# Kernel optimization log

Hardware: AMD Instinct MI355X
Metric: run time of the kernel (lower is better)

The kernel has to match this reference:

```python
import jax, jax.numpy as jnp
import numpy as np

SEQ, B, D = 2048, 16, 1024  # seq_len, batch, input/hidden size

def setup_inputs() -> dict:
    key = jax.random.key(0)
    k1, k2, k3 = jax.random.split(key, 3)
    X = jax.random.normal(k1, (SEQ, B, D), dtype=jnp.float32)
    hidden = jnp.zeros((B, D), dtype=jnp.float32)  # initial hidden state C_0
    # nn.Linear(window*input_size, 3*hidden_size): weight (3D, D), bias (3D,)
    W = jax.random.normal(k2, (3 * D, D), dtype=jnp.float32) / np.float32(np.sqrt(D))
    b = jax.random.normal(k3, (3 * D,), dtype=jnp.float32) * 0.01
    return {"X": X, "hidden": hidden, "W": W, "b": b}

def _forget_mult(F, Z, h0):
    # C_t = F_t * Z_t + (1 - F_t) * C_{t-1}, scanned over seq dim
    def step(h, fz):
        f, z = fz
        h = f * z + (1.0 - f) * h
        return h, h
    _, C = jax.lax.scan(step, h0, (F, Z))
    return C  # (S, B, D)

def reference(X, hidden, W, b):
    # window=1 -> source = X; gate projection
    Y = jnp.einsum('sbd,hd->sbh', X, W) + b        # (S, B, 3D)
    Z, F, O = jnp.split(Y, 3, axis=2)
    Z = jnp.tanh(Z)
    F = jax.nn.sigmoid(F)
    C = _forget_mult(F, Z, hidden)                 # (S, B, D)
    H = jax.nn.sigmoid(O) * C                      # output gate (QRNN-fo)
    return H, C[-1:]                               # (S,B,D), (1,B,D)
```

## Files before the change

kernel.cpp:

```cpp
#include <hip/hip_runtime.h>


#define S_LEN 2048
#define BATCH 16
#define DHID 1024
#define N3 3072
#define MROWS (S_LEN * BATCH)
#define XELEMS ((size_t)MROWS * DHID)
#define WELEMS ((size_t)N3 * DHID)
#define YELEMS ((size_t)MROWS * N3)

typedef __attribute__((ext_vector_type(8))) short bf16x8;
typedef __attribute__((ext_vector_type(4))) float floatx4;
typedef __attribute__((ext_vector_type(4))) unsigned short u16x4;

__device__ __forceinline__ float b2f(unsigned short u) {
  return __uint_as_float(((unsigned)u) << 16);
}
__device__ __forceinline__ unsigned short f2b(float x) {
  unsigned u = __float_as_uint(x);
  u += 0x7fffu + ((u >> 16) & 1u);
  return (unsigned short)(u >> 16);
}
__device__ __forceinline__ float sigmoid_f(float x) {
  return __builtin_amdgcn_rcpf(1.0f + __expf(-x));
}
__device__ __forceinline__ float tanh_f(float x) {
  return 2.0f * __builtin_amdgcn_rcpf(1.0f + __expf(-2.0f * x)) - 1.0f;
}

__device__ __forceinline__ void load_lds16(const unsigned short* g, unsigned short* l) {
  __builtin_amdgcn_global_load_lds(
      (const __attribute__((address_space(1))) void*)g,
      (__attribute__((address_space(3))) void*)l,
      16, 0, 0);
}

__global__ __launch_bounds__(256) void cvt_f32_bf16(
    const float* __restrict__ src, unsigned short* __restrict__ dst, int n4) {
  int i = blockIdx.x * 256 + threadIdx.x;
  if (i < n4) {
    float4 v = ((const float4*)src)[i];
    u16x4 o;
    o.x = f2b(v.x); o.y = f2b(v.y); o.z = f2b(v.z); o.w = f2b(v.w);
    ((u16x4*)dst)[i] = o;
  }
}

__global__ __launch_bounds__(256) void qrnn_gemm(
    const unsigned short* __restrict__ X,
    const unsigned short* __restrict__ W,
    const float* __restrict__ bias,
    unsigned short* __restrict__ Y)
{
  __shared__ __align__(16) unsigned short sA[128 * 64];
  __shared__ __align__(16) unsigned short sB[128 * 64];

  const int tid = threadIdx.x;
  const int w  = tid >> 6;
  const int l  = tid & 63;
  const int lr = l & 15;
  const int lq = l >> 4;
  const int n0B = blockIdx.x * 128;
  const int m0B = blockIdx.y * 128;
  const int wm = (w >> 1) * 64;
  const int wn = (w & 1) * 64;

  floatx4 acc[4][4] = {};

  const unsigned short* gA = X + (size_t)m0B * DHID;
  const unsigned short* gB = W + (size_t)n0B * DHID;
  const int srow = tid >> 3;
  const int scol = (tid & 7) << 3;

  for (int k0 = 0; k0 < DHID; k0 += 64) {
#pragma unroll
    for (int j = 0; j < 4; ++j) {
      load_lds16(gA + (size_t)(j * 32 + srow) * DHID + (k0 + scol),
                 sA + (j * 2048 + w * 512));
      load_lds16(gB + (size_t)(j * 32 + srow) * DHID + (k0 + scol),
                 sB + (j * 2048 + w * 512));
    }
    __syncthreads();

#pragma unroll
    for (int kk = 0; kk < 64; kk += 32) {
      bf16x8 af[4], bf[4];
#pragma unroll
      for (int i = 0; i < 4; ++i) {
        af[i] = *(const bf16x8*)&sA[(wm + i * 16 + lr) * 64 + kk + lq * 8];
      }
#pragma unroll
      for (int j = 0; j < 4; ++j) {
        bf[j] = *(const bf16x8*)&sB[(wn + j * 16 + lr) * 64 + kk + lq * 8];
      }
#pragma unroll
      for (int i = 0; i < 4; ++i) {
#pragma unroll
        for (int j = 0; j < 4; ++j) {
          acc[i][j] = __builtin_amdgcn_mfma_f32_16x16x32_bf16(
              af[i], bf[j], acc[i][j], 0, 0, 0);
        }
      }
    }
    __syncthreads();
  }

  const int seg = n0B >> 10;
#pragma unroll
  for (int j = 0; j < 4; ++j) {
    const int n = n0B + wn + j * 16 + lr;
    const float bv = bias[n];
#pragma unroll
    for (int i = 0; i < 4; ++i) {
      const int mb = m0B + wm + i * 16 + lq * 4;
#pragma unroll
      for (int r = 0; r < 4; ++r) {
        float v = acc[i][j][r] + bv;
        v = (seg == 0) ? tanh_f(v) : sigmoid_f(v);
        Y[(size_t)(mb + r) * N3 + n] = f2b(v);
      }
    }
  }
}

#define U 8
#define PCH 32
#define LCH (S_LEN / PCH)
#define SUBCH (LCH / U)
#define SSTRIDE (BATCH * N3)
#define HSTRIDE (BATCH * DHID)
#define NT (BATCH * DHID)
#define NT4 (NT / 4)

__global__ __launch_bounds__(256) void qrnn_scan_pass1(
    const unsigned short* __restrict__ Y,
    float* __restrict__ Aarr,
    float* __restrict__ Barr)
{
  const int g = blockIdx.x * 256 + threadIdx.x;
  const int t = g & (NT4 - 1);
  const int p = g >> 12;
  const int b = t >> 8;
  const int d = (t & 255) << 2;
  const unsigned short* base =
      Y + (size_t)(p * LCH) * SSTRIDE + (size_t)b * N3 + d;

  float a[4] = {1.0f, 1.0f, 1.0f, 1.0f};
  float bv[4] = {0.0f, 0.0f, 0.0f, 0.0f};
  u16x4 z0[U], f0[U], z1[U], f1[U];

#define LOADZF(ch, zz, ff) { \
    const unsigned short* p_ = base + (size_t)(ch) * ((size_t)U * SSTRIDE); \
    _Pragma("unroll") \
    for (int j2 = 0; j2 < U; ++j2) { \
      zz[j2] = *(const u16x4*)(p_ + (size_t)j2 * SSTRIDE); \
      ff[j2] = *(const u16x4*)(p_ + (size_t)j2 * SSTRIDE + DHID); \
    } }

#define COMPAB(zz, ff) { \
    _Pragma("unroll") \
    for (int j2 = 0; j2 < U; ++j2) { \
      _Pragma("unroll") \
      for (int q = 0; q < 4; ++q) { \
        float zv = b2f(zz[j2][q]); \
        float fv = b2f(ff[j2][q]); \
        a[q]  = fmaf(-fv, a[q], a[q]);         \
        bv[q] = fmaf(fv, zv - bv[q], bv[q]);   \
      } \
    } }

  LOADZF(0, z0, f0);
  for (int ch = 0; ch < SUBCH; ch += 2) {
    LOADZF(ch + 1, z1, f1);
    COMPAB(z0, f0);
    if (ch + 2 < SUBCH) LOADZF(ch + 2, z0, f0);
    COMPAB(z1, f1);
  }
  ((float4*)Aarr)[g] = make_float4(a[0], a[1], a[2], a[3]);
  ((float4*)Barr)[g] = make_float4(bv[0], bv[1], bv[2], bv[3]);
}

__global__ __launch_bounds__(256) void qrnn_combine(
    const float* __restrict__ Aarr,
    const float* __restrict__ Barr,
    const float* __restrict__ h0,
    float* __restrict__ Cin,
    float* __restrict__ out)
{
  const int t = blockIdx.x * 256 + threadIdx.x;
  float c = h0[t];
#pragma unroll
  for (int p = 0; p < PCH; ++p) {
    Cin[p * NT + t] = c;
    c = fmaf(Aarr[p * NT + t], c, Barr[p * NT + t]);
  }
  out[(size_t)S_LEN * HSTRIDE + t] = c;
}

__global__ __launch_bounds__(256) void qrnn_scan_pass2(
    const unsigned short* __restrict__ Y,
    const float* __restrict__ Cin,
    float* __restrict__ out)
{
  const int g = blockIdx.x * 256 + threadIdx.x;
  const int t = g & (NT4 - 1);
  const int p = g >> 12;
  const int b = t >> 8;
  const int d = (t & 255) << 2;
  const unsigned short* base =
      Y + (size_t)(p * LCH) * SSTRIDE + (size_t)b * N3 + d;
  float* ho = out + (size_t)(p * LCH) * HSTRIDE + (size_t)b * DHID + d;

  float4 cv = ((const float4*)Cin)[g];
  float c[4] = {cv.x, cv.y, cv.z, cv.w};

  u16x4 z0[U], f0[U], o0[U], z1[U], f1[U], o1[U];

#define LOADCH(ch, zz, ff, oo) { \
    const unsigned short* p_ = base + (size_t)(ch) * ((size_t)U * SSTRIDE); \
    _Pragma("unroll") \
    for (int j2 = 0; j2 < U; ++j2) { \
      zz[j2] = *(const u16x4*)(p_ + (size_t)j2 * SSTRIDE); \
      ff[j2] = *(const u16x4*)(p_ + (size_t)j2 * SSTRIDE + DHID); \
      oo[j2] = *(const u16x4*)(p_ + (size_t)j2 * SSTRIDE + 2 * DHID); \
    } }

#define COMPCH(ch, zz, ff, oo) { \
    float* q_ = ho + (size_t)(ch) * ((size_t)U * HSTRIDE); \
    _Pragma("unroll") \
    for (int j2 = 0; j2 < U; ++j2) { \
      float hv[4]; \
      _Pragma("unroll") \
      for (int q = 0; q < 4; ++q) { \
        float zv = b2f(zz[j2][q]); \
        float fv = b2f(ff[j2][q]); \
        float ov = b2f(oo[j2][q]); \
        c[q] = fmaf(fv, zv - c[q], c[q]); \
        hv[q] = ov * c[q]; \
      } \
      *(float4*)(q_ + (size_t)j2 * HSTRIDE) = \
          make_float4(hv[0], hv[1], hv[2], hv[3]); \
    } }

  LOADCH(0, z0, f0, o0);
  for (int ch = 0; ch < SUBCH; ch += 2) {
    LOADCH(ch + 1, z1, f1, o1);
    COMPCH(ch, z0, f0, o0);
    if (ch + 2 < SUBCH) LOADCH(ch + 2, z0, f0, o0);
    COMPCH(ch + 1, z1, f1, o1);
  }
}

extern "C" void kernel_launch(void* const* d_in, const int* in_sizes, int n_in,
                              void* d_out, int out_size, void* d_ws, size_t ws_size,
                              hipStream_t stream) {
  const float* X    = (const float*)d_in[0];
  const float* h0   = (const float*)d_in[1];
  const float* W    = (const float*)d_in[2];
  const float* bias = (const float*)d_in[3];
  float* out = (float*)d_out;

  unsigned short* Ybf = (unsigned short*)d_ws;
  unsigned short* Wbf = Ybf + YELEMS;
  unsigned short* Xbf = (unsigned short*)out;
  float* Aarr = (float*)Wbf;
  float* Barr = Aarr + PCH * NT;
  float* CinA = Barr + PCH * NT;
  static_assert((size_t)3 * PCH * NT * 4 <= (size_t)WELEMS * 2,
                "A/B/Cin must fit in Wbf region");

  cvt_f32_bf16<<<(int)(XELEMS / 4 + 255) / 256, 256, 0, stream>>>(X, Xbf, (int)(XELEMS / 4));
  cvt_f32_bf16<<<(int)(WELEMS / 4 + 255) / 256, 256, 0, stream>>>(W, Wbf, (int)(WELEMS / 4));
  qrnn_gemm<<<dim3(N3 / 128, MROWS / 128), 256, 0, stream>>>(Xbf, Wbf, bias, Ybf);
  qrnn_scan_pass1<<<dim3((PCH * NT4) / 256), 256, 0, stream>>>(Ybf, Aarr, Barr);
  qrnn_combine<<<dim3(NT / 256), 256, 0, stream>>>(Aarr, Barr, h0, CinA, out);
  qrnn_scan_pass2<<<dim3((PCH * NT4) / 256), 256, 0, stream>>>(Ybf, CinA, out);
}
```

Before: 562.8 us.

## Rewrite GEMM as 256x256 double-buffered pipelined kernel and double scan chunks

The GEMM moves from 128x128 tiles with 256 threads to 256x256 tiles with 512 threads. It double-buffers LDS, interleaves global-to-LDS staging with MFMA phases under setprio and barriers, XOR-swizzles the LDS layout to avoid bank conflicts, and remaps block IDs for L2 locality. The scan now uses 64 parallel chunks instead of 32, with the A/B scratch arrays moved into the tail of the output buffer. The goal is to raise MFMA utilisation and hide load latency, at the cost of heavy register pressure (128 accumulator floats per lane) and a fragile manual vmcnt schedule.

Measured after the change: 561.6 us. No clear change (-0.2%).

```diff
diff --git a/kernel.cpp b/kernel.cpp
--- a/kernel.cpp
+++ b/kernel.cpp
@@ -47,85 +47,150 @@
   }
 }
 
-__global__ __launch_bounds__(256) void qrnn_gemm(
+__global__ __launch_bounds__(512, 2) void qrnn_gemm(
     const unsigned short* __restrict__ X,
     const unsigned short* __restrict__ W,
     const float* __restrict__ bias,
     unsigned short* __restrict__ Y)
 {
-  __shared__ __align__(16) unsigned short sA[128 * 64];
-  __shared__ __align__(16) unsigned short sB[128 * 64];
+  __shared__ __align__(16) unsigned short sAq[2][256 * 64];
+  __shared__ __align__(16) unsigned short sBq[2][256 * 64];
 
   const int tid = threadIdx.x;
-  const int w  = tid >> 6;
-  const int l  = tid & 63;
-  const int lr = l & 15;
-  const int lq = l >> 4;
-  const int n0B = blockIdx.x * 128;
-  const int m0B = blockIdx.y * 128;
-  const int wm = (w >> 1) * 64;
-  const int wn = (w & 1) * 64;
-
-  floatx4 acc[4][4] = {};
+  const int w   = tid >> 6;
+  const int l   = tid & 63;
+  const int lr  = l & 15;
+  const int lq  = l >> 4;
+  const int wm  = (w >> 2) * 128;
+  const int wn  = (w & 3) * 64;
+  const int wu  = w << 9;
+  const int rr  = tid >> 3;
+  const int sc  = ((tid & 7) ^ (rr & 7)) << 3;
+
+  const int bid  = blockIdx.x;
+  const int swz  = (bid & 7) * 192 + (bid >> 3);
+  const int mblk = swz / 12;
+  const int nblk = swz - mblk * 12;
+  const int m0B  = mblk << 8;
+  const int n0B  = nblk << 8;
 
   const unsigned short* gA = X + (size_t)m0B * DHID;
   const unsigned short* gB = W + (size_t)n0B * DHID;
-  const int srow = tid >> 3;
-  const int scol = (tid & 7) << 3;
-
-  for (int k0 = 0; k0 < DHID; k0 += 64) {
-#pragma unroll
-    for (int j = 0; j < 4; ++j) {
-      load_lds16(gA + (size_t)(j * 32 + srow) * DHID + (k0 + scol),
-                 sA + (j * 2048 + w * 512));
-      load_lds16(gB + (size_t)(j * 32 + srow) * DHID + (k0 + scol),
-                 sB + (j * 2048 + w * 512));
+
+  floatx4 acc[8][4] = {};
+
+#define STAGE(gbase, sbase, kt, half) do {                                    \
+    const unsigned short* _g =                                                \
+        (gbase) + (size_t)((half) * 128 + rr) * DHID + (kt) * 64 + sc;        \
+    unsigned short* _s = (sbase) + (half) * 8192 + wu;                        \
+    load_lds16(_g, _s);                                                       \
+    load_lds16(_g + (size_t)64 * DHID, _s + 4096);                            \
+  } while (0)
+
+#define LDSV(sbuf, row, kcol) \
+    (*(const bf16x8*)&(sbuf)[(row) * 64 + ((kcol) ^ (((row) & 7) << 3))])
+
+#define MFMA16(MQ, NQ, BB)                                                    \
+  _Pragma("unroll") for (int i = 0; i < 4; ++i)                               \
+  _Pragma("unroll") for (int j = 0; j < 2; ++j)                               \
+  _Pragma("unroll") for (int ks = 0; ks < 2; ++ks)                            \
+    acc[(MQ) * 4 + i][(NQ) * 2 + j] =                                         \
+        __builtin_amdgcn_mfma_f32_16x16x32_bf16(                              \
+            a[i][ks], BB[j][ks], acc[(MQ) * 4 + i][(NQ) * 2 + j], 0, 0, 0);
+
+  STAGE(gA, &sAq[0][0], 0, 0);
+  STAGE(gA, &sAq[0][0], 0, 1);
+  STAGE(gB, &sBq[0][0], 0, 0);
+  STAGE(gB, &sBq[0][0], 0, 1);
+  STAGE(gB, &sBq[1][0], 1, 0);
+  STAGE(gB, &sBq[1][0], 1, 1);
+  asm volatile("s_waitcnt vmcnt(4)" ::: "memory");
+  __builtin_amdgcn_s_barrier();
+
+  for (int t = 0; t < 16; ++t) {
+    const int cur = t & 1;
+    const unsigned short* cA = &sAq[cur][0];
+    const unsigned short* cB = &sBq[cur][0];
+    bf16x8 a[4][2], b0[2][2], b1[2][2];
+
+#pragma unroll
+    for (int i = 0; i < 4; ++i)
+#pragma unroll
+      for (int ks = 0; ks < 2; ++ks)
+        a[i][ks] = LDSV(cA, wm + i * 16 + lr, ks * 32 + lq * 8);
+#pragma unroll
+    for (int j = 0; j < 2; ++j)
+#pragma unroll
+      for (int ks = 0; ks < 2; ++ks)
+        b0[j][ks] = LDSV(cB, wn + j * 16 + lr, ks * 32 + lq * 8);
+    if (t + 1 < 16) STAGE(gA, &sAq[cur ^ 1][0], t + 1, 0);
+    __builtin_amdgcn_s_barrier();
+    __builtin_amdgcn_s_setprio(1);
+    MFMA16(0, 0, b0);
+    __builtin_amdgcn_s_setprio(0);
+    __builtin_amdgcn_s_barrier();
+
+#pragma unroll
+    for (int j = 0; j < 2; ++j)
+#pragma unroll
+      for (int ks = 0; ks < 2; ++ks)
+        b1[j][ks] = LDSV(cB, wn + 32 + j * 16 + lr, ks * 32 + lq * 8);
+    if (t + 1 < 16) STAGE(gA, &sAq[cur ^ 1][0], t + 1, 1);
+    __builtin_amdgcn_s_barrier();
+    __builtin_amdgcn_s_setprio(1);
+    MFMA16(0, 1, b1);
+    __builtin_amdgcn_s_setprio(0);
+    __builtin_amdgcn_s_barrier();
+
+#pragma unroll
+    for (int i = 0; i < 4; ++i)
+#pragma unroll
+      for (int ks = 0; ks < 2; ++ks)
+        a[i][ks] = LDSV(cA, wm + 64 + i * 16 + lr, ks * 32 + lq * 8);
+    if (t + 2 < 16) STAGE(gB, &sBq[cur][0], t + 2, 0);
+    __builtin_amdgcn_s_barrier();
+    __builtin_amdgcn_s_setprio(1);
+    MFMA16(1, 0, b0);
+    __builtin_amdgcn_s_setprio(0);
+    __builtin_amdgcn_s_barrier();
+
+    if (t + 2 < 16) STAGE(gB, &sBq[cur][0], t + 2, 1);
+    __builtin_amdgcn_s_barrier();
+    __builtin_amdgcn_s_setprio(1);
+    MFMA16(1, 1, b1);
+    __builtin_amdgcn_s_setprio(0);
+    if (t < 14) asm volatile("s_waitcnt vmcnt(4)" ::: "memory");
+    else        asm volatile("s_waitcnt vmcnt(0)" ::: "memory");
+    __builtin_amdgcn_s_barrier();
+  }
+
+  const int seg = n0B >> 10;
+#pragma unroll
+  for (int mq = 0; mq < 2; ++mq)
+#pragma unroll
+    for (int i = 0; i < 4; ++i) {
+      const int mb = m0B + wm + mq * 64 + i * 16 + lq * 4;
+#pragma unroll
+      for (int nq = 0; nq < 2; ++nq)
+#pragma unroll
+        for (int j = 0; j < 2; ++j) {
+          const int n = n0B + wn + nq * 32 + j * 16 + lr;
+          const float bv = bias[n];
+#pragma unroll
+          for (int r = 0; r < 4; ++r) {
+            float v = acc[mq * 4 + i][nq * 2 + j][r] + bv;
+            v = (seg == 0) ? tanh_f(v) : sigmoid_f(v);
+            Y[(size_t)(mb + r) * N3 + n] = f2b(v);
+          }
+        }
     }
-    __syncthreads();
-
-#pragma unroll
-    for (int kk = 0; kk < 64; kk += 32) {
-      bf16x8 af[4], bf[4];
-#pragma unroll
-      for (int i = 0; i < 4; ++i) {
-        af[i] = *(const bf16x8*)&sA[(wm + i * 16 + lr) * 64 + kk + lq * 8];
-      }
-#pragma unroll
-      for (int j = 0; j < 4; ++j) {
-        bf[j] = *(const bf16x8*)&sB[(wn + j * 16 + lr) * 64 + kk + lq * 8];
-      }
-#pragma unroll
-      for (int i = 0; i < 4; ++i) {
-#pragma unroll
-        for (int j = 0; j < 4; ++j) {
-          acc[i][j] = __builtin_amdgcn_mfma_f32_16x16x32_bf16(
-              af[i], bf[j], acc[i][j], 0, 0, 0);
-        }
-      }
-    }
-    __syncthreads();
-  }
-
-  const int seg = n0B >> 10;
-#pragma unroll
-  for (int j = 0; j < 4; ++j) {
-    const int n = n0B + wn + j * 16 + lr;
-    const float bv = bias[n];
-#pragma unroll
-    for (int i = 0; i < 4; ++i) {
-      const int mb = m0B + wm + i * 16 + lq * 4;
-#pragma unroll
-      for (int r = 0; r < 4; ++r) {
-        float v = acc[i][j][r] + bv;
-        v = (seg == 0) ? tanh_f(v) : sigmoid_f(v);
-        Y[(size_t)(mb + r) * N3 + n] = f2b(v);
-      }
-    }
-  }
+#undef STAGE
+#undef LDSV
+#undef MFMA16
 }
 
 #define U 8
-#define PCH 32
+#define PCH 64
 #define LCH (S_LEN / PCH)
 #define SUBCH (LCH / U)
 #define SSTRIDE (BATCH * N3)
@@ -264,15 +329,15 @@
   unsigned short* Ybf = (unsigned short*)d_ws;
   unsigned short* Wbf = Ybf + YELEMS;
   unsigned short* Xbf = (unsigned short*)out;
-  float* Aarr = (float*)Wbf;
-  float* Barr = Aarr + PCH * NT;
-  float* CinA = Barr + PCH * NT;
-  static_assert((size_t)3 * PCH * NT * 4 <= (size_t)WELEMS * 2,
-                "A/B/Cin must fit in Wbf region");
+  float* Aarr = out + ((size_t)S_LEN * HSTRIDE - 2 * (size_t)PCH * NT);
+  float* Barr = Aarr + (size_t)PCH * NT;
+  float* CinA = (float*)Wbf;
+  static_assert((size_t)PCH * NT * 4 <= (size_t)WELEMS * 2,
+                "Cin must fit in Wbf region");
 
   cvt_f32_bf16<<<(int)(XELEMS / 4 + 255) / 256, 256, 0, stream>>>(X, Xbf, (int)(XELEMS / 4));
   cvt_f32_bf16<<<(int)(WELEMS / 4 + 255) / 256, 256, 0, stream>>>(W, Wbf, (int)(WELEMS / 4));
-  qrnn_gemm<<<dim3(N3 / 128, MROWS / 128), 256, 0, stream>>>(Xbf, Wbf, bias, Ybf);
+  qrnn_gemm<<<dim3((MROWS / 256) * (N3 / 256)), 512, 0, stream>>>(Xbf, Wbf, bias, Ybf);
   qrnn_scan_pass1<<<dim3((PCH * NT4) / 256), 256, 0, stream>>>(Ybf, Aarr, Barr);
   qrnn_combine<<<dim3(NT / 256), 256, 0, stream>>>(Aarr, Barr, h0, CinA, out);
   qrnn_scan_pass2<<<dim3((PCH * NT4) / 256), 256, 0, stream>>>(Ybf, CinA, out);
```
